# Kernel tuning notes

Measured on AMD Instinct MI355X. Metric: run time of the kernel, lower is better.

The kernel has to match this reference:

```python
import jax, jax.numpy as jnp
import numpy as np

B, S, H, T, F, L = 32, 512, 1024, 100, 512, 5  # batch, seq, hidden, num_topics, topic_hidden, n_langs
EPS = 1e-5


def _layernorm(x, g, b):
    mu = jnp.mean(x, axis=-1, keepdims=True)
    var = jnp.mean((x - mu) ** 2, axis=-1, keepdims=True)
    return (x - mu) * jax.lax.rsqrt(var + EPS) * g + b


def setup_inputs() -> dict:
    key = jax.random.key(0)
    ks = jax.random.split(key, 16)
    sc = 0.02
    return {
        "sequence_output": jax.random.normal(ks[0], (B, S, H), dtype=jnp.float32),
        "attention_mask": jnp.ones((B, S), dtype=jnp.float32),
        "language_ids": jax.random.randint(ks[1], (B,), 0, L, dtype=jnp.int32),
        "lda_features": jax.random.uniform(ks[2], (B, T), dtype=jnp.float32),
        # per-language adapter params (stacked over L)
        "W1": jax.random.normal(ks[3], (L, H, H), dtype=jnp.float32) * sc,
        "b1": jnp.zeros((L, H), dtype=jnp.float32),
        "g1": jnp.ones((L, H), dtype=jnp.float32),
        "beta1": jnp.zeros((L, H), dtype=jnp.float32),
        "W2": jax.random.normal(ks[4], (L, H, H), dtype=jnp.float32) * sc,
        "b2": jnp.zeros((L, H), dtype=jnp.float32),
        # topic fusion params
        "Wf": jax.random.normal(ks[5], (H + T, F), dtype=jnp.float32) * sc,
        "bf": jnp.zeros((F,), dtype=jnp.float32),
        "gf": jnp.ones((F,), dtype=jnp.float32),
        "betaf": jnp.zeros((F,), dtype=jnp.float32),
    }


def reference(sequence_output, attention_mask, language_ids, lda_features,
              W1, b1, g1, beta1, W2, b2, Wf, bf, gf, betaf):
    # Apply every language adapter to the full batch, then mask-accumulate
    # (faithful to the original anti-pattern).
    adapted = jnp.zeros_like(sequence_output)
    for lang in range(L):
        h = jnp.einsum("bsh,he->bse", sequence_output, W1[lang]) + b1[lang]
        h = jax.nn.relu(_layernorm(h, g1[lang], beta1[lang]))
        h = jnp.einsum("bsh,he->bse", h, W2[lang]) + b2[lang]
        lang_mask = (language_ids == lang).astype(sequence_output.dtype)[:, None, None]
        adapted = adapted + lang_mask * h
    # masked mean pool over sequence
    masked = adapted * attention_mask[:, :, None]
    pooled = masked.sum(axis=1) / attention_mask.sum(axis=1)[:, None]  # [B, H]
    combined = jnp.concatenate([pooled, lda_features], axis=-1)        # [B, H+T]
    fused = _layernorm(combined @ Wf + bf, gf, betaf)
    return jax.nn.relu(fused)  # dropout is identity in eval
```

## Files before the change

kernel.cpp:

```cpp
#include <hip/hip_runtime.h>
#include <hip/hip_bf16.h>
#include <stdint.h>

#define Bq 32
#define Sq 512
#define Hq 1024
#define Tq 100
#define Fq 512
#define Lq 5
#define EPSq 1e-5f

typedef float fx4 __attribute__((ext_vector_type(4)));
typedef __bf16 bfx8 __attribute__((ext_vector_type(8)));
typedef unsigned short u16x8 __attribute__((ext_vector_type(8)));

static __device__ __forceinline__ unsigned short f2bf(float f) {
  unsigned int u = __builtin_bit_cast(unsigned int, f);
  return (unsigned short)((u + 0x7fffu + ((u >> 16) & 1u)) >> 16);
}
static __device__ __forceinline__ float bf2f(unsigned short s) {
  return __builtin_bit_cast(float, ((unsigned int)s) << 16);
}
static __device__ __forceinline__ void gl_lds16(const void* g, void* l) {
  __builtin_amdgcn_global_load_lds(
      (const __attribute__((address_space(1))) unsigned int*)(uintptr_t)g,
      (__attribute__((address_space(3))) unsigned int*)(uintptr_t)l,
      16, 0, 0);
}

__global__ void k_prep(const float* __restrict__ seq, unsigned short* __restrict__ seqbf,
                       const float* __restrict__ w1, unsigned short* __restrict__ w1t) {
  int blk = blockIdx.x;
  int tid = threadIdx.x;
  if (blk < 8192) {
    int i = blk * 256 + tid;
    const float4* p = (const float4*)seq + (size_t)i * 2;
    float4 a = p[0], b = p[1];
    u16x8 o;
    o[0] = f2bf(a.x); o[1] = f2bf(a.y); o[2] = f2bf(a.z); o[3] = f2bf(a.w);
    o[4] = f2bf(b.x); o[5] = f2bf(b.y); o[6] = f2bf(b.z); o[7] = f2bf(b.w);
    *((u16x8*)seqbf + i) = o;
  } else {
    __shared__ float t[32][33];
    int bb = blk - 8192;
    int l = bb >> 10; int rem = bb & 1023; int tr = rem >> 5; int tc = rem & 31;
    const float* src = w1 + (size_t)l * Hq * Hq;
    unsigned short* dst = w1t + (size_t)l * Hq * Hq;
    int tx = tid & 31, ty = tid >> 5;
#pragma unroll
    for (int p = 0; p < 4; p++)
      t[ty + 8 * p][tx] = src[(size_t)(tr * 32 + ty + 8 * p) * Hq + tc * 32 + tx];
    __syncthreads();
#pragma unroll
    for (int p = 0; p < 4; p++)
      dst[(size_t)(tc * 32 + ty + 8 * p) * Hq + tr * 32 + tx] = f2bf(t[tx][ty + 8 * p]);
  }
}

__global__ __launch_bounds__(256) void k_gemm1(const unsigned short* __restrict__ seqbf,
                                               const unsigned short* __restrict__ w1t,
                                               const float* __restrict__ b1,
                                               const int* __restrict__ lid,
                                               unsigned short* __restrict__ h1bf) {
  __shared__ short sA[3][128 * 32];
  __shared__ short sB[3][128 * 32];
  int bid = blockIdx.x;
  int g = bid & 127; int tn = bid >> 7;
  int b = g >> 2; int tm = g & 3;
  int lang = lid[b];
  const unsigned short* Ab = seqbf + (size_t)b * Sq * Hq + (size_t)tm * 128 * Hq;
  const unsigned short* Bb = w1t + (size_t)lang * Hq * Hq + (size_t)tn * 128 * Hq;

  int tid = threadIdx.x;
  int lane = tid & 63; int wid = tid >> 6;
  int wr = wid >> 1, wc = wid & 1;
  int fr = lane & 15;
  int q = lane >> 4;
  int key = ((fr >> 1) & 7) << 4;

  const unsigned short* gA[2]; const unsigned short* gB[2]; int dst[2];
#pragma unroll
  for (int j = 0; j < 2; j++) {
    int p = (tid + j * 256) * 16;
    int l = p ^ ((p >> 3) & 0x70);
    int R = l >> 6, qa = (l >> 4) & 3;
    gA[j] = Ab + (size_t)R * Hq + qa * 8;
    gB[j] = Bb + (size_t)R * Hq + qa * 8;
    dst[j] = p;
  }

  int aOff[4], bOff[4];
#pragma unroll
  for (int i = 0; i < 4; i++) {
    aOff[i] = ((wr * 64 + i * 16 + fr) * 64 + q * 16) ^ key;
    bOff[i] = ((wc * 64 + i * 16 + fr) * 64 + q * 16) ^ key;
  }

  fx4 acc[4][4];
#pragma unroll
  for (int m = 0; m < 4; m++)
#pragma unroll
    for (int n = 0; n < 4; n++) acc[m][n] = (fx4){0.f, 0.f, 0.f, 0.f};

#pragma unroll
  for (int j = 0; j < 2; j++) {
    gl_lds16(gA[j], (char*)sA[0] + dst[j]);
    gl_lds16(gB[j], (char*)sB[0] + dst[j]);
  }
#pragma unroll
  for (int j = 0; j < 2; j++) {
    gl_lds16(gA[j] + 32, (char*)sA[1] + dst[j]);
    gl_lds16(gB[j] + 32, (char*)sB[1] + dst[j]);
  }

  for (int kt = 0; kt < 32; kt++) {
    int cur = kt % 3;
    if (kt < 31)
      asm volatile("s_waitcnt vmcnt(4) lgkmcnt(0)\n\ts_barrier" ::: "memory");
    else
      asm volatile("s_waitcnt vmcnt(0) lgkmcnt(0)\n\ts_barrier" ::: "memory");
    if (kt < 30) {
      int nb = (kt + 2) % 3;
      int ko = (kt + 2) * 32;
#pragma unroll
      for (int j = 0; j < 2; j++) {
        gl_lds16(gA[j] + ko, (char*)sA[nb] + dst[j]);
        gl_lds16(gB[j] + ko, (char*)sB[nb] + dst[j]);
      }
    }
    const char* cA = (const char*)sA[cur];
    const char* cB = (const char*)sB[cur];
    bfx8 af[4], bfr[4];
#pragma unroll
    for (int m = 0; m < 4; m++) af[m] = *(const bfx8*)(cA + aOff[m]);
#pragma unroll
    for (int n = 0; n < 4; n++) bfr[n] = *(const bfx8*)(cB + bOff[n]);
    __builtin_amdgcn_s_setprio(1);
#pragma unroll
    for (int m = 0; m < 4; m++)
#pragma unroll
      for (int n = 0; n < 4; n++)
        acc[m][n] = __builtin_amdgcn_mfma_f32_16x16x32_bf16(af[m], bfr[n], acc[m][n], 0, 0, 0);
    __builtin_amdgcn_s_setprio(0);
  }

  unsigned short* Cb = h1bf + (size_t)b * Sq * Hq;
  float bv[4];
#pragma unroll
  for (int n = 0; n < 4; n++)
    bv[n] = b1[lang * Hq + tn * 128 + wc * 64 + n * 16 + fr];
  int r0 = q * 4;
#pragma unroll
  for (int m = 0; m < 4; m++) {
#pragma unroll
    for (int n = 0; n < 4; n++) {
      int col = tn * 128 + wc * 64 + n * 16 + fr;
#pragma unroll
      for (int r = 0; r < 4; r++) {
        int row = tm * 128 + wr * 64 + m * 16 + r0 + r;
        Cb[(size_t)row * Hq + col] = f2bf(acc[m][n][r] + bv[n]);
      }
    }
  }
}

__global__ __launch_bounds__(256) void k_ln_pool(const unsigned short* __restrict__ h1bf,
                                                 const float* __restrict__ g1,
                                                 const float* __restrict__ be1,
                                                 const float* __restrict__ mask,
                                                 const int* __restrict__ lid,
                                                 float* __restrict__ partial) {
  __shared__ float sacc[4][1024];
  int blk = blockIdx.x; int b = blk >> 3; int ch = blk & 7;
  int tid = threadIdx.x; int lane = tid & 63; int w = tid >> 6;
  int lang = lid[b];
  int e0 = lane * 8;
  int e1 = 512 + lane * 8;

  const float4* gp = (const float4*)(g1 + (size_t)lang * Hq);
  const float4* bp = (const float4*)(be1 + (size_t)lang * Hq);
  float4 ga0 = gp[lane * 2], ga1 = gp[lane * 2 + 1];
  float4 gb0 = gp[128 + lane * 2], gb1 = gp[129 + lane * 2];
  float4 ba0 = bp[lane * 2], ba1 = bp[lane * 2 + 1];
  float4 bb0 = bp[128 + lane * 2], bb1 = bp[129 + lane * 2];
  float gA[8] = {ga0.x, ga0.y, ga0.z, ga0.w, ga1.x, ga1.y, ga1.z, ga1.w};
  float gB[8] = {gb0.x, gb0.y, gb0.z, gb0.w, gb1.x, gb1.y, gb1.z, gb1.w};
  float bA[8] = {ba0.x, ba0.y, ba0.z, ba0.w, ba1.x, ba1.y, ba1.z, ba1.w};
  float bB[8] = {bb0.x, bb0.y, bb0.z, bb0.w, bb1.x, bb1.y, bb1.z, bb1.w};

  float acc0[8] = {0, 0, 0, 0, 0, 0, 0, 0}, acc1[8] = {0, 0, 0, 0, 0, 0, 0, 0};

  for (int i = 0; i < 16; i++) {
    int s = ch * 64 + w * 16 + i;
    const unsigned short* rowp = h1bf + ((size_t)b * Sq + s) * Hq;
    u16x8 va = *(const u16x8*)(rowp + e0);
    u16x8 vb = *(const u16x8*)(rowp + e1);
    float xa[8], xb[8];
    float sum = 0.f, sq = 0.f;
#pragma unroll
    for (int j = 0; j < 8; j++) {
      xa[j] = bf2f(va[j]); sum += xa[j]; sq += xa[j] * xa[j];
      xb[j] = bf2f(vb[j]); sum += xb[j]; sq += xb[j] * xb[j];
    }
#pragma unroll
    for (int off = 1; off < 64; off <<= 1) {
      sum += __shfl_xor(sum, off, 64);
      sq += __shfl_xor(sq, off, 64);
    }
    float mu = sum * (1.f / Hq);
    float var = sq * (1.f / Hq) - mu * mu;
    float rstd = rsqrtf(var + EPSq);
    float mw = mask[b * Sq + s];
#pragma unroll
    for (int j = 0; j < 8; j++) {
      float y0 = fmaxf((xa[j] - mu) * rstd * gA[j] + bA[j], 0.f);
      float y1 = fmaxf((xb[j] - mu) * rstd * gB[j] + bB[j], 0.f);
      acc0[j] += mw * y0;
      acc1[j] += mw * y1;
    }
  }
#pragma unroll
  for (int j = 0; j < 8; j++) {
    sacc[w][e0 + j] = acc0[j];
    sacc[w][e1 + j] = acc1[j];
  }
  __syncthreads();
  int e = tid * 4;
#pragma unroll
  for (int j = 0; j < 4; j++)
    partial[(size_t)blk * Hq + e + j] =
        sacc[0][e + j] + sacc[1][e + j] + sacc[2][e + j] + sacc[3][e + j];
}

__global__ void k_reduce_pool(const float* __restrict__ partial, const float* __restrict__ mask,
                              float* __restrict__ pooled) {
  __shared__ float wsum[4];
  int b = blockIdx.x; int tid = threadIdx.x;
  float mv = mask[b * Sq + tid] + mask[b * Sq + 256 + tid];
#pragma unroll
  for (int off = 1; off < 64; off <<= 1) mv += __shfl_xor(mv, off, 64);
  if ((tid & 63) == 0) wsum[tid >> 6] = mv;
  __syncthreads();
  float inv = 1.0f / (wsum[0] + wsum[1] + wsum[2] + wsum[3]);
  int e = tid * 4;
#pragma unroll
  for (int j = 0; j < 4; j++) {
    float s = 0.f;
#pragma unroll
    for (int c = 0; c < 8; c++) s += partial[((size_t)b * 8 + c) * Hq + e + j];
    pooled[b * Hq + e + j] = s * inv;
  }
}

__global__ __launch_bounds__(256) void k_gemm2p(const float* __restrict__ pooled,
                                                const float* __restrict__ w2,
                                                const int* __restrict__ lid,
                                                float* __restrict__ g2part) {
  __shared__ float pl[256];
  int blk = blockIdx.x;
  int b = blk >> 3; int ch = (blk >> 2) & 1; int ks = blk & 3;
  int tid = threadIdx.x;
  int lang = lid[b];
  pl[tid] = pooled[b * Hq + ks * 256 + tid];
  __syncthreads();
  int col = ch * 512 + tid * 2;
  const float* W = w2 + (size_t)lang * Hq * Hq + (size_t)ks * 256 * Hq + col;
  float a0 = 0.f, a1 = 0.f;
  for (int e0 = 0; e0 < 256; e0 += 8) {
    float2 w[8];
#pragma unroll
    for (int j = 0; j < 8; j++) w[j] = *(const float2*)(W + (size_t)(e0 + j) * Hq);
#pragma unroll
    for (int j = 0; j < 8; j++) { float c = pl[e0 + j]; a0 += c * w[j].x; a1 += c * w[j].y; }
  }
  float2* dst = (float2*)(g2part + ((size_t)(b * 4 + ks) * Hq) + col);
  *dst = make_float2(a0, a1);
}

__global__ __launch_bounds__(256) void k_gemm2red(const float* __restrict__ g2part,
                                                  const float* __restrict__ b2,
                                                  const int* __restrict__ lid,
                                                  float* __restrict__ pooledf) {
  int b = blockIdx.x; int tid = threadIdx.x;
  int lang = lid[b];
  int col = tid * 4;
  float4 acc = *(const float4*)(b2 + (size_t)lang * Hq + col);
#pragma unroll
  for (int ks = 0; ks < 4; ks++) {
    float4 p = *(const float4*)(g2part + ((size_t)(b * 4 + ks) * Hq) + col);
    acc.x += p.x; acc.y += p.y; acc.z += p.z; acc.w += p.w;
  }
  *(float4*)(pooledf + (size_t)b * Hq + col) = acc;
}

__global__ __launch_bounds__(256) void k_fpart(const float* __restrict__ pooledf,
                                               const float* __restrict__ lda,
                                               const float* __restrict__ wf,
                                               float* __restrict__ fpart) {
  __shared__ float sc[128];
  int blk = blockIdx.x;
  int b = blk / 9, ks = blk % 9;
  int tid = threadIdx.x;
  int klen = (ks < 8) ? 128 : 100;
  int kbase = (ks < 8) ? ks * 128 : Hq;
  if (tid < klen) sc[tid] = (ks < 8) ? pooledf[b * Hq + kbase + tid] : lda[b * Tq + tid];
  __syncthreads();
  const float* W = wf + (size_t)kbase * Fq + tid * 2;
  float a0 = 0.f, a1 = 0.f;
  int k0 = 0;
  for (; k0 + 8 <= klen; k0 += 8) {
    float2 w[8];
#pragma unroll
    for (int j = 0; j < 8; j++) w[j] = *(const float2*)(W + (size_t)(k0 + j) * Fq);
#pragma unroll
    for (int j = 0; j < 8; j++) { float c = sc[k0 + j]; a0 += c * w[j].x; a1 += c * w[j].y; }
  }
  for (; k0 < klen; k0++) {
    float2 w = *(const float2*)(W + (size_t)k0 * Fq);
    float c = sc[k0];
    a0 += c * w.x; a1 += c * w.y;
  }
  float2* dst = (float2*)(fpart + (size_t)blk * Fq + tid * 2);
  *dst = make_float2(a0, a1);
}

__global__ __launch_bounds__(512) void k_final2(const float* __restrict__ fpart,
                                                const float* __restrict__ bff,
                                                const float* __restrict__ gf,
                                                const float* __restrict__ betaf,
                                                float* __restrict__ out) {
  __shared__ float rsum[8], rsq[8];
  int b = blockIdx.x; int tid = threadIdx.x;
  float acc = bff[tid];
#pragma unroll
  for (int ks = 0; ks < 9; ks++) acc += fpart[((size_t)b * 9 + ks) * Fq + tid];
  float s = acc, q = acc * acc;
#pragma unroll
  for (int off = 1; off < 64; off <<= 1) {
    s += __shfl_xor(s, off, 64);
    q += __shfl_xor(q, off, 64);
  }
  int w = tid >> 6, lane = tid & 63;
  if (lane == 0) { rsum[w] = s; rsq[w] = q; }
  __syncthreads();
  float S = 0.f, Q = 0.f;
#pragma unroll
  for (int i = 0; i < 8; i++) { S += rsum[i]; Q += rsq[i]; }
  float mu = S * (1.f / Fq);
  float var = Q * (1.f / Fq) - mu * mu;
  float y = (acc - mu) * rsqrtf(var + EPSq) * gf[tid] + betaf[tid];
  y = fmaxf(y, 0.f);
  out[b * Fq + tid] = y;
}

extern "C" void kernel_launch(void* const* d_in, const int* in_sizes, int n_in,
                              void* d_out, int out_size, void* d_ws, size_t ws_size,
                              hipStream_t stream) {
  const float* seq = (const float*)d_in[0];
  const float* mask = (const float*)d_in[1];
  const int* lid = (const int*)d_in[2];
  const float* lda = (const float*)d_in[3];
  const float* W1 = (const float*)d_in[4];
  const float* b1 = (const float*)d_in[5];
  const float* g1 = (const float*)d_in[6];
  const float* be1 = (const float*)d_in[7];
  const float* W2 = (const float*)d_in[8];
  const float* b2 = (const float*)d_in[9];
  const float* Wf = (const float*)d_in[10];
  const float* bff = (const float*)d_in[11];
  const float* gf = (const float*)d_in[12];
  const float* betaf = (const float*)d_in[13];
  float* out = (float*)d_out;

  char* ws = (char*)d_ws;
  unsigned short* seqbf = (unsigned short*)(ws);
  unsigned short* w1t = (unsigned short*)(ws + 33554432);
  unsigned short* h1bf = (unsigned short*)(ws + 44040192);
  float* partial = (float*)(ws + 77594624);
  float* pooled = (float*)(ws + 78643200);
  float* pooledf = (float*)(ws + 78774272);
  float* g2part = (float*)(ws + 78905344);
  float* fpart = (float*)(ws + 79429632);

  k_prep<<<13312, 256, 0, stream>>>(seq, seqbf, W1, w1t);
  k_gemm1<<<1024, 256, 0, stream>>>(seqbf, w1t, b1, lid, h1bf);
  k_ln_pool<<<256, 256, 0, stream>>>(h1bf, g1, be1, mask, lid, partial);
  k_reduce_pool<<<32, 256, 0, stream>>>(partial, mask, pooled);
  k_gemm2p<<<256, 256, 0, stream>>>(pooled, W2, lid, g2part);
  k_gemm2red<<<32, 256, 0, stream>>>(g2part, b2, lid, pooledf);
  k_fpart<<<288, 256, 0, stream>>>(pooledf, lda, Wf, fpart);
  k_final2<<<32, 512, 0, stream>>>(fpart, bff, gf, betaf, out);
}
```

Measured before the change: 112.5 us.

## Enlarge gemm1 tile to 256x256 with 8 waves and 4-stage LDS pipeline

The first GEMM goes from 128x128 tiles with 4 waves to 256x256 tiles with 8 waves, each wave computing 128x64 of output. The LDS ring grows from 3 to 4 stages, with loads issued three steps ahead. The goal is to raise arithmetic intensity and cut global/LDS traffic per FLOP, and to hide more load latency. In exchange the grid shrinks to 256 blocks on a 256-CU device, 128 KB of LDS per block allows only one block per CU, and the 8x4 accumulators raise register pressure.

```diff
diff --git a/kernel.cpp b/kernel.cpp
--- a/kernel.cpp
+++ b/kernel.cpp
@@ -57,90 +57,91 @@
   }
 }
 
-__global__ __launch_bounds__(256) void k_gemm1(const unsigned short* __restrict__ seqbf,
-                                               const unsigned short* __restrict__ w1t,
-                                               const float* __restrict__ b1,
-                                               const int* __restrict__ lid,
-                                               unsigned short* __restrict__ h1bf) {
-  __shared__ short sA[3][128 * 32];
-  __shared__ short sB[3][128 * 32];
+__global__ __launch_bounds__(512, 2) void k_gemm1(const unsigned short* __restrict__ seqbf,
+                                                  const unsigned short* __restrict__ w1t,
+                                                  const float* __restrict__ b1,
+                                                  const int* __restrict__ lid,
+                                                  unsigned short* __restrict__ h1bf) {
+  __shared__ short sA[4][256 * 32];
+  __shared__ short sB[4][256 * 32];
   int bid = blockIdx.x;
-  int g = bid & 127; int tn = bid >> 7;
-  int b = g >> 2; int tm = g & 3;
+  int g = bid & 63; int tn = bid >> 6;
+  int b = g >> 1; int tm = g & 1;
   int lang = lid[b];
-  const unsigned short* Ab = seqbf + (size_t)b * Sq * Hq + (size_t)tm * 128 * Hq;
-  const unsigned short* Bb = w1t + (size_t)lang * Hq * Hq + (size_t)tn * 128 * Hq;
+  const unsigned short* Ab = seqbf + (size_t)b * Sq * Hq + (size_t)tm * 256 * Hq;
+  const unsigned short* Bb = w1t + (size_t)lang * Hq * Hq + (size_t)tn * 256 * Hq;
 
   int tid = threadIdx.x;
   int lane = tid & 63; int wid = tid >> 6;
-  int wr = wid >> 1, wc = wid & 1;
+  int wr = wid >> 2, wc = wid & 3;
   int fr = lane & 15;
   int q = lane >> 4;
   int key = ((fr >> 1) & 7) << 4;
 
-  const unsigned short* gA[2]; const unsigned short* gB[2]; int dst[2];
+  const unsigned short* gA[2]; const unsigned short* gB[2]; int dstOff[2];
 #pragma unroll
   for (int j = 0; j < 2; j++) {
-    int p = (tid + j * 256) * 16;
+    int p = (tid + j * 512) * 16;
     int l = p ^ ((p >> 3) & 0x70);
     int R = l >> 6, qa = (l >> 4) & 3;
     gA[j] = Ab + (size_t)R * Hq + qa * 8;
     gB[j] = Bb + (size_t)R * Hq + qa * 8;
-    dst[j] = p;
-  }
-
-  int aOff[4], bOff[4];
-#pragma unroll
-  for (int i = 0; i < 4; i++) {
-    aOff[i] = ((wr * 64 + i * 16 + fr) * 64 + q * 16) ^ key;
-    bOff[i] = ((wc * 64 + i * 16 + fr) * 64 + q * 16) ^ key;
-  }
-
-  fx4 acc[4][4];
-#pragma unroll
-  for (int m = 0; m < 4; m++)
+    dstOff[j] = p;
+  }
+
+  int aOff[8], bOff[4];
+#pragma unroll
+  for (int m = 0; m < 8; m++)
+    aOff[m] = ((wr * 128 + m * 16 + fr) * 64 + q * 16) ^ key;
+#pragma unroll
+  for (int n = 0; n < 4; n++)
+    bOff[n] = ((wc * 64 + n * 16 + fr) * 64 + q * 16) ^ key;
+
+  fx4 acc[8][4];
+#pragma unroll
+  for (int m = 0; m < 8; m++)
 #pragma unroll
     for (int n = 0; n < 4; n++) acc[m][n] = (fx4){0.f, 0.f, 0.f, 0.f};
 
 #pragma unroll
-  for (int j = 0; j < 2; j++) {
-    gl_lds16(gA[j], (char*)sA[0] + dst[j]);
-    gl_lds16(gB[j], (char*)sB[0] + dst[j]);
-  }
-#pragma unroll
-  for (int j = 0; j < 2; j++) {
-    gl_lds16(gA[j] + 32, (char*)sA[1] + dst[j]);
-    gl_lds16(gB[j] + 32, (char*)sB[1] + dst[j]);
-  }
-
-  for (int kt = 0; kt < 32; kt++) {
-    int cur = kt % 3;
-    if (kt < 31)
+  for (int s = 0; s < 3; s++) {
+#pragma unroll
+    for (int j = 0; j < 2; j++) {
+      gl_lds16(gA[j] + s * 32, (char*)sA[s] + dstOff[j]);
+      gl_lds16(gB[j] + s * 32, (char*)sB[s] + dstOff[j]);
+    }
+  }
+
+  for (int hs = 0; hs < 32; hs++) {
+    int cur = hs & 3;
+    if (hs < 30)
+      asm volatile("s_waitcnt vmcnt(8) lgkmcnt(0)\n\ts_barrier" ::: "memory");
+    else if (hs == 30)
       asm volatile("s_waitcnt vmcnt(4) lgkmcnt(0)\n\ts_barrier" ::: "memory");
     else
       asm volatile("s_waitcnt vmcnt(0) lgkmcnt(0)\n\ts_barrier" ::: "memory");
-    if (kt < 30) {
-      int nb = (kt + 2) % 3;
-      int ko = (kt + 2) * 32;
+    if (hs <= 28) {
+      int slot = (hs + 3) & 3;
+      int ko = (hs + 3) * 32;
 #pragma unroll
       for (int j = 0; j < 2; j++) {
-        gl_lds16(gA[j] + ko, (char*)sA[nb] + dst[j]);
-        gl_lds16(gB[j] + ko, (char*)sB[nb] + dst[j]);
+        gl_lds16(gA[j] + ko, (char*)sA[slot] + dstOff[j]);
+        gl_lds16(gB[j] + ko, (char*)sB[slot] + dstOff[j]);
       }
     }
     const char* cA = (const char*)sA[cur];
     const char* cB = (const char*)sB[cur];
-    bfx8 af[4], bfr[4];
-#pragma unroll
-    for (int m = 0; m < 4; m++) af[m] = *(const bfx8*)(cA + aOff[m]);
-#pragma unroll
-    for (int n = 0; n < 4; n++) bfr[n] = *(const bfx8*)(cB + bOff[n]);
+    bfx8 bf[4], af[8];
+#pragma unroll
+    for (int n = 0; n < 4; n++) bf[n] = *(const bfx8*)(cB + bOff[n]);
+#pragma unroll
+    for (int m = 0; m < 8; m++) af[m] = *(const bfx8*)(cA + aOff[m]);
     __builtin_amdgcn_s_setprio(1);
 #pragma unroll
-    for (int m = 0; m < 4; m++)
+    for (int m = 0; m < 8; m++)
 #pragma unroll
       for (int n = 0; n < 4; n++)
-        acc[m][n] = __builtin_amdgcn_mfma_f32_16x16x32_bf16(af[m], bfr[n], acc[m][n], 0, 0, 0);
+        acc[m][n] = __builtin_amdgcn_mfma_f32_16x16x32_bf16(af[m], bf[n], acc[m][n], 0, 0, 0);
     __builtin_amdgcn_s_setprio(0);
   }
 
@@ -148,16 +149,16 @@
   float bv[4];
 #pragma unroll
   for (int n = 0; n < 4; n++)
-    bv[n] = b1[lang * Hq + tn * 128 + wc * 64 + n * 16 + fr];
+    bv[n] = b1[lang * Hq + tn * 256 + wc * 64 + n * 16 + fr];
   int r0 = q * 4;
 #pragma unroll
-  for (int m = 0; m < 4; m++) {
+  for (int m = 0; m < 8; m++) {
 #pragma unroll
     for (int n = 0; n < 4; n++) {
-      int col = tn * 128 + wc * 64 + n * 16 + fr;
+      int col = tn * 256 + wc * 64 + n * 16 + fr;
 #pragma unroll
       for (int r = 0; r < 4; r++) {
-        int row = tm * 128 + wr * 64 + m * 16 + r0 + r;
+        int row = tm * 256 + wr * 128 + m * 16 + r0 + r;
         Cb[(size_t)row * Hq + col] = f2bf(acc[m][n][r] + bv[n]);
       }
     }
@@ -383,7 +384,7 @@
   float* fpart = (float*)(ws + 79429632);
 
   k_prep<<<13312, 256, 0, stream>>>(seq, seqbf, W1, w1t);
-  k_gemm1<<<1024, 256, 0, stream>>>(seqbf, w1t, b1, lid, h1bf);
+  k_gemm1<<<256, 512, 0, stream>>>(seqbf, w1t, b1, lid, h1bf);
   k_ln_pool<<<256, 256, 0, stream>>>(h1bf, g1, be1, mask, lid, partial);
   k_reduce_pool<<<32, 256, 0, stream>>>(partial, mask, pooled);
   k_gemm2p<<<256, 256, 0, stream>>>(pooled, W2, lid, g2part);
```

After: 101.6 us. 1.11x faster.
